# Performance work log

Hardware: AMD Instinct MI355X
Metric: run time of the kernel (lower is better)

## Reference

```python
import jax, jax.numpy as jnp
import numpy as np

TAU = 0.125
VTH = 1.0
V_R = 0.0
ALPHA = 2.0  # ATan surrogate sharpness (spikingjelly default)


@jax.custom_vjp
def surrogate(x):
    # Heaviside forward
    return (x >= 0).astype(x.dtype)


def _sur_fwd(x):
    return surrogate(x), x


def _sur_bwd(x, g):
    # ATan surrogate gradient: alpha/2 / (1 + (pi/2 * alpha * x)^2)
    sg = (ALPHA / 2.0) / (1.0 + (jnp.pi / 2.0 * ALPHA * x) ** 2)
    return (g * sg,)


surrogate.defvjp(_sur_fwd, _sur_bwd)


def setup_inputs() -> dict:
    key = jax.random.key(0)
    x = jax.random.normal(key, (32, 4096, 256), dtype=jnp.float32)
    return {"x": x}


def reference(x):
    # x: [B, N, T]; time is the last axis, scanned sequentially.
    xT = jnp.moveaxis(x, -1, 0)  # [T, B, N]

    def step(u, xt):
        u = u * TAU + xt                      # leaky integrate
        s = surrogate(u - VTH)                # spike (heaviside fwd)
        s_det = jax.lax.stop_gradient(s)      # torch uses s.detach() in reset
        u_next = (1.0 - s_det) * u + s_det * V_R  # hard reset
        return u_next, s

    u0 = jnp.zeros_like(xT[0])
    _, out = jax.lax.scan(step, u0, xT)       # out: [T, B, N]
    return jnp.moveaxis(out, 0, -1)           # [B, N, T]
```

## Files before the change

kernel.cpp:

```cpp
#include <hip/hip_runtime.h>


typedef float f32x4 __attribute__((ext_vector_type(4)));

constexpr int   T    = 256;
constexpr int   TV   = T / 4;
constexpr int   CT   = 32;
constexpr int   CV   = CT / 4;
constexpr int   NCH  = T / CT;
constexpr int   SEQB = 256;
constexpr int   RP   = CT + 1;
constexpr float TAU  = 0.125f;
constexpr float VTH  = 1.0f;

__global__ __launch_bounds__(256)
void lif_fwd(const f32x4* __restrict__ x, f32x4* __restrict__ out, int nseq) {
    __shared__ float lds[SEQB * RP];

    const int tid  = threadIdx.x;
    const int bseq = blockIdx.x * SEQB;

    float u = 0.0f;

    for (int ch = 0; ch < NCH; ++ch) {
        const size_t cbase = (size_t)bseq * TV + ch * CV;

        #pragma unroll
        for (int j = 0; j < CV; ++j) {
            int f = j * SEQB + tid;
            int s = f >> 3;
            int k = f & 7;
            f32x4 v = x[cbase + (size_t)s * TV + k - (size_t)0 * TV];
            float* d = &lds[s * RP + k * 4];
            d[0] = v.x; d[1] = v.y; d[2] = v.z; d[3] = v.w;
        }
        __syncthreads();

        #pragma unroll
        for (int t = 0; t < CT; ++t) {
            float xv = lds[tid * RP + t];
            u = u * TAU + xv;
            bool b = (u >= VTH);
            lds[tid * RP + t] = b ? 1.0f : 0.0f;
            u = b ? 0.0f : u;
        }
        __syncthreads();

        #pragma unroll
        for (int j = 0; j < CV; ++j) {
            int f = j * SEQB + tid;
            int s = f >> 3;
            int k = f & 7;
            const float* p = &lds[s * RP + k * 4];
            f32x4 v; v.x = p[0]; v.y = p[1]; v.z = p[2]; v.w = p[3];
            out[cbase + (size_t)s * TV + k] = v;
        }
        __syncthreads();
    }
}

extern "C" void kernel_launch(void* const* d_in, const int* in_sizes, int n_in,
                              void* d_out, int out_size, void* d_ws, size_t ws_size,
                              hipStream_t stream) {
    const float* x = (const float*)d_in[0];
    float* out = (float*)d_out;

    int nseq = in_sizes[0] / T;
    int grid = nseq / SEQB;

    lif_fwd<<<grid, SEQB, 0, stream>>>(
        (const f32x4*)x, (f32x4*)out, nseq);
}
```

Measured before the change: 46.04 us.

## Double-buffer LDS and prefetch next time chunk while scanning current chunk

```diff
diff --git a/kernel.cpp b/kernel.cpp
--- a/kernel.cpp
+++ b/kernel.cpp
@@ -8,54 +8,67 @@
 constexpr int   CT   = 32;
 constexpr int   CV   = CT / 4;
 constexpr int   NCH  = T / CT;
-constexpr int   SEQB = 256;
+constexpr int   SEQB = 64;
 constexpr int   RP   = CT + 1;
 constexpr float TAU  = 0.125f;
 constexpr float VTH  = 1.0f;
 
-__global__ __launch_bounds__(256)
+__global__ __launch_bounds__(64)
 void lif_fwd(const f32x4* __restrict__ x, f32x4* __restrict__ out, int nseq) {
-    __shared__ float lds[SEQB * RP];
+    __shared__ float lds[2 * SEQB * RP];
+    float* bufA = lds;
+    float* bufB = lds + SEQB * RP;
 
     const int tid  = threadIdx.x;
+    const int srow = tid >> 3;
+    const int k    = tid & 7;
     const int bseq = blockIdx.x * SEQB;
 
+    #pragma unroll
+    for (int j = 0; j < CV; ++j) {
+        f32x4 v = x[(size_t)(bseq + j*8 + srow) * TV + k];
+        float* d = &bufA[(j*8 + srow) * RP + k*4];
+        d[0]=v.x; d[1]=v.y; d[2]=v.z; d[3]=v.w;
+    }
+    __syncthreads();
+
     float u = 0.0f;
-
+    #pragma unroll
     for (int ch = 0; ch < NCH; ++ch) {
-        const size_t cbase = (size_t)bseq * TV + ch * CV;
-
-        #pragma unroll
-        for (int j = 0; j < CV; ++j) {
-            int f = j * SEQB + tid;
-            int s = f >> 3;
-            int k = f & 7;
-            f32x4 v = x[cbase + (size_t)s * TV + k - (size_t)0 * TV];
-            float* d = &lds[s * RP + k * 4];
-            d[0] = v.x; d[1] = v.y; d[2] = v.z; d[3] = v.w;
+        f32x4 r[CV];
+        if (ch + 1 < NCH) {
+            #pragma unroll
+            for (int j = 0; j < CV; ++j)
+                r[j] = x[(size_t)(bseq + j*8 + srow) * TV + (ch+1)*CV + k];
         }
-        __syncthreads();
 
         #pragma unroll
         for (int t = 0; t < CT; ++t) {
-            float xv = lds[tid * RP + t];
+            float xv = bufA[tid * RP + t];
             u = u * TAU + xv;
             bool b = (u >= VTH);
-            lds[tid * RP + t] = b ? 1.0f : 0.0f;
+            bufA[tid * RP + t] = b ? 1.0f : 0.0f;
             u = b ? 0.0f : u;
         }
         __syncthreads();
 
         #pragma unroll
         for (int j = 0; j < CV; ++j) {
-            int f = j * SEQB + tid;
-            int s = f >> 3;
-            int k = f & 7;
-            const float* p = &lds[s * RP + k * 4];
-            f32x4 v; v.x = p[0]; v.y = p[1]; v.z = p[2]; v.w = p[3];
-            out[cbase + (size_t)s * TV + k] = v;
+            const float* p = &bufA[(j*8 + srow) * RP + k*4];
+            f32x4 v; v.x=p[0]; v.y=p[1]; v.z=p[2]; v.w=p[3];
+            out[(size_t)(bseq + j*8 + srow) * TV + ch*CV + k] = v;
+        }
+        if (ch + 1 < NCH) {
+            #pragma unroll
+            for (int j = 0; j < CV; ++j) {
+                float* d = &bufB[(j*8 + srow) * RP + k*4];
+                f32x4 v = r[j];
+                d[0]=v.x; d[1]=v.y; d[2]=v.z; d[3]=v.w;
+            }
         }
         __syncthreads();
+
+        float* tmp = bufA; bufA = bufB; bufB = tmp;
     }
 }
 
```

Result: faster. 44.74 us (-2.8%).

## Split time axis into quarters with warm-up recurrence and register prefetch

Applied to the files above, without the earlier changes.

```diff
diff --git a/kernel.cpp b/kernel.cpp
--- a/kernel.cpp
+++ b/kernel.cpp
@@ -5,57 +5,78 @@
 
 constexpr int   T    = 256;
 constexpr int   TV   = T / 4;
-constexpr int   CT   = 32;
-constexpr int   CV   = CT / 4;
-constexpr int   NCH  = T / CT;
-constexpr int   SEQB = 256;
-constexpr int   RP   = CT + 1;
+constexpr int   NQ   = 4;
+constexpr int   QV   = TV / NQ;
+constexpr int   PH   = 4;
+constexpr int   PV   = QV / PH;
+constexpr int   WV   = 4;
+constexpr int   RP   = PV * 4 + 1;
+constexpr int   ROWS = 64;
+constexpr int   BAND = ROWS * RP;
 constexpr float TAU  = 0.125f;
 constexpr float VTH  = 1.0f;
 
-__global__ __launch_bounds__(256)
+__global__ __launch_bounds__(256, 4)
 void lif_fwd(const f32x4* __restrict__ x, f32x4* __restrict__ out, int nseq) {
-    __shared__ float lds[SEQB * RP];
+    __shared__ float lds[NQ * BAND];
 
     const int tid  = threadIdx.x;
-    const int bseq = blockIdx.x * SEQB;
+    const int q    = tid >> 6;
+    const int s    = tid & 63;
+    const int bseq = blockIdx.x * ROWS;
+    const f32x4* xq = x + (size_t)(bseq + s) * TV + q * QV;
 
     float u = 0.0f;
 
-    for (int ch = 0; ch < NCH; ++ch) {
-        const size_t cbase = (size_t)bseq * TV + ch * CV;
+    if (q > 0) {
+        f32x4 w[WV];
+        #pragma unroll
+        for (int j = 0; j < WV; ++j) w[j] = xq[j - WV];
+        #pragma unroll
+        for (int j = 0; j < WV; ++j) {
+            #pragma unroll
+            for (int e = 0; e < 4; ++e) {
+                u = u * TAU + w[j][e];
+                u = (u >= VTH) ? 0.0f : u;
+            }
+        }
+    }
 
+    f32x4 cur[PV], nxt[PV];
+    #pragma unroll
+    for (int j = 0; j < PV; ++j) cur[j] = xq[j];
+
+    float* myband = &lds[q * BAND + s * RP];
+    const int r = tid >> 2, k = tid & 3;
+
+    #pragma unroll
+    for (int p = 0; p < PH; ++p) {
+        if (p + 1 < PH) {
+            #pragma unroll
+            for (int j = 0; j < PV; ++j) nxt[j] = xq[(p + 1) * PV + j];
+        }
         #pragma unroll
-        for (int j = 0; j < CV; ++j) {
-            int f = j * SEQB + tid;
-            int s = f >> 3;
-            int k = f & 7;
-            f32x4 v = x[cbase + (size_t)s * TV + k - (size_t)0 * TV];
-            float* d = &lds[s * RP + k * 4];
-            d[0] = v.x; d[1] = v.y; d[2] = v.z; d[3] = v.w;
+        for (int j = 0; j < PV; ++j) {
+            #pragma unroll
+            for (int e = 0; e < 4; ++e) {
+                u = u * TAU + cur[j][e];
+                bool b = (u >= VTH);
+                myband[j * 4 + e] = b ? 1.0f : 0.0f;
+                u = b ? 0.0f : u;
+            }
         }
         __syncthreads();
-
         #pragma unroll
-        for (int t = 0; t < CT; ++t) {
-            float xv = lds[tid * RP + t];
-            u = u * TAU + xv;
-            bool b = (u >= VTH);
-            lds[tid * RP + t] = b ? 1.0f : 0.0f;
-            u = b ? 0.0f : u;
+        for (int m = 0; m < NQ; ++m) {
+            const float* pp = &lds[m * BAND + r * RP + k * 4];
+            f32x4 v; v.x = pp[0]; v.y = pp[1]; v.z = pp[2]; v.w = pp[3];
+            out[(size_t)(bseq + r) * TV + m * QV + p * PV + k] = v;
         }
         __syncthreads();
-
-        #pragma unroll
-        for (int j = 0; j < CV; ++j) {
-            int f = j * SEQB + tid;
-            int s = f >> 3;
-            int k = f & 7;
-            const float* p = &lds[s * RP + k * 4];
-            f32x4 v; v.x = p[0]; v.y = p[1]; v.z = p[2]; v.w = p[3];
-            out[cbase + (size_t)s * TV + k] = v;
+        if (p + 1 < PH) {
+            #pragma unroll
+            for (int j = 0; j < PV; ++j) cur[j] = nxt[j];
         }
-        __syncthreads();
     }
 }
 
@@ -66,8 +87,8 @@
     float* out = (float*)d_out;
 
     int nseq = in_sizes[0] / T;
-    int grid = nseq / SEQB;
+    int grid = nseq / ROWS;
 
-    lif_fwd<<<grid, SEQB, 0, stream>>>(
+    lif_fwd<<<grid, 256, 0, stream>>>(
         (const f32x4*)x, (f32x4*)out, nseq);
 }
```

New measurement: 60.45 us. 1.31x slower.
